# Performance work log

Measured on AMD Instinct MI355X. Metric: run time of the kernel, lower is better.

## Reference

```python
import jax, jax.numpy as jnp
import numpy as np

EPS = 1e-12  # torch F.normalize clamps the norm at 1e-12

def _l2norm(v, axis):
    n = jnp.sqrt(jnp.sum(v * v, axis=axis, keepdims=True))
    return v / jnp.maximum(n, EPS)

def setup_inputs() -> dict:
    key = jax.random.key(0)
    k1, k2, k3, k4 = jax.random.split(key, 4)
    N, C, H, W, K = 64, 64, 64, 64, 128
    alpha = 1.0
    x = jax.random.normal(k1, (N, C, H, W), dtype=jnp.float32)
    centroids = jax.random.uniform(k2, (K, C), dtype=jnp.float32)
    # conv is initialized from centroids (2*alpha*c, -alpha*||c||) but is an
    # independent parameter after init; keep the init relationship for realism.
    conv_w = 2.0 * alpha * centroids
    conv_b = -alpha * jnp.sqrt(jnp.sum(centroids * centroids, axis=1))
    return {"x": x, "centroids": centroids, "conv_w": conv_w, "conv_b": conv_b}

def reference(x, centroids, conv_w, conv_b):
    N, C, H, W = x.shape
    K = centroids.shape[0]
    # L2-normalize descriptors along channel dim
    xn = _l2norm(x, axis=1)                                   # [N,C,H,W]
    # 1x1 conv == per-pixel linear map C->K
    logits = jnp.einsum('nchw,kc->nkhw', xn, conv_w) + conv_b[None, :, None, None]
    sa = jax.nn.softmax(logits.reshape(N, K, H * W), axis=1)  # [N,K,HW]
    xf = xn.reshape(N, C, H * W)                              # [N,C,HW]
    # vlad[n,k,c] = sum_l sa[n,k,l] * (xf[n,c,l] - centroids[k,c])
    #            = (sa @ xf^T)[n,k,c] - sum_l sa[n,k,l] * centroids[k,c]
    vlad = jnp.einsum('nkl,ncl->nkc', sa, xf) - sa.sum(axis=-1)[:, :, None] * centroids[None]
    vlad = _l2norm(vlad, axis=2)            # intra-normalization per cluster
    vlad = vlad.reshape(N, K * C)
    vlad = _l2norm(vlad, axis=1)            # global L2 normalization
    return vlad
```

## Files before the change

### kernel.cpp

```cpp
#include <hip/hip_runtime.h>
#include <math.h>

#define NIMG   64
#define CDIM   64
#define HWPX   4096
#define KCL    128
#define TL     32
#define SHIFT  10.0f
#define RSQRT128 0.08838834764831845f

#define XP_S 72
#define XC_S 40
#define PH_S 40

typedef __attribute__((ext_vector_type(8))) short short8;
typedef __attribute__((ext_vector_type(4))) float f32x4;

#define MFMA(a, b, c) __builtin_amdgcn_mfma_f32_16x16x32_bf16((a), (b), (c), 0, 0, 0)

#define PERM_HI16 0x07060302u

#define BAR() do {                                          \
    asm volatile("s_waitcnt lgkmcnt(0)" ::: "memory");      \
    __builtin_amdgcn_s_barrier();                           \
    __builtin_amdgcn_sched_barrier(0);                      \
} while (0)

template <int NP>
__global__ __launch_bounds__(256, 2)
void netvlad_main(const float* __restrict__ x,
                  const float* __restrict__ conv_w,
                  const float* __restrict__ conv_b,
                  float* __restrict__ vout,
                  float* __restrict__ asout,
                  int use_atomic)
{
    constexpr int PIXPART = HWPX / NP;
    constexpr int NCHUNK  = PIXPART / TL;

    __shared__ __align__(16) short xp_hi[2][TL * XP_S], xp_lo[2][TL * XP_S];
    __shared__ __align__(16) short xc[2][CDIM * XC_S];
    __shared__ __align__(16) short ph[KCL * PH_S];
    __shared__ __align__(8) float2 redA2[2][4 * 16];
    __shared__ __align__(8) float2 sumP2[4 * 16];

    const int t   = threadIdx.x;
    const int w   = t >> 6;
    const int l   = t & 63;
    const int l15 = l & 15, l4 = l >> 4;
    const int n    = blockIdx.x / NP;
    const int part = blockIdx.x - n * NP;
    const int p_s  = t & 31;
    const int sg   = t >> 5;
    const int slot = 2 * (p_s & 15) + (p_s >> 4);

    short8 wh[2][2], wl[2][2];
    #pragma unroll
    for (int kt = 0; kt < 2; ++kt) {
        const int krow = (2 * w + kt) * 16 + l15;
        #pragma unroll
        for (int ks = 0; ks < 2; ++ks) {
            const float4* wp = (const float4*)(conv_w + krow * CDIM + ks * 32 + l4 * 8);
            float4 wa = wp[0], wb = wp[1];
            float wv[8] = {wa.x, wa.y, wa.z, wa.w, wb.x, wb.y, wb.z, wb.w};
            #pragma unroll
            for (int j = 0; j < 8; ++j) {
                unsigned u = __builtin_bit_cast(unsigned, wv[j]);
                wh[kt][ks][j] = (short)(u >> 16);
                float hf = __builtin_bit_cast(float, u & 0xffff0000u);
                wl[kt][ks][j] = (short)(__builtin_bit_cast(unsigned, wv[j] - hf) >> 16);
            }
        }
    }
    float cbr[2][4];
    #pragma unroll
    for (int kt = 0; kt < 2; ++kt)
        #pragma unroll
        for (int i = 0; i < 4; ++i)
            cbr[kt][i] = conv_b[(2 * w + kt) * 16 + l4 * 4 + i] - SHIFT;

    f32x4 acc2[2][4];
    #pragma unroll
    for (int a = 0; a < 2; ++a)
        #pragma unroll
        for (int b = 0; b < 4; ++b) acc2[a][b] = (f32x4)0.0f;
    float asr[2][4];
    #pragma unroll
    for (int a = 0; a < 2; ++a)
        #pragma unroll
        for (int i = 0; i < 4; ++i) asr[a][i] = 0.f;

    const float* xbase = x + (size_t)n * CDIM * HWPX + part * PIXPART;

    float xv[8];

    auto stage = [&](int buf) {
        float ssq = 0.f;
        #pragma unroll
        for (int j = 0; j < 8; ++j) ssq += xv[j] * xv[j];
        ssq += __shfl_xor(ssq, 32);
        float ssq_hi = __shfl_xor(ssq, 16);
        if (l < 16) redA2[buf][w * 16 + l15] = make_float2(ssq, ssq_hi);

        unsigned uh[4], ul[4];
        #pragma unroll
        for (int jp = 0; jp < 4; ++jp) {
            const unsigned u0 = __builtin_bit_cast(unsigned, xv[2 * jp]);
            const unsigned u1 = __builtin_bit_cast(unsigned, xv[2 * jp + 1]);
            uh[jp] = __builtin_amdgcn_perm(u1, u0, PERM_HI16);
            const float h0 = __builtin_bit_cast(float, u0 & 0xffff0000u);
            const float h1 = __builtin_bit_cast(float, u1 & 0xffff0000u);
            const unsigned lo0 = __builtin_bit_cast(unsigned, xv[2 * jp] - h0);
            const unsigned lo1 = __builtin_bit_cast(unsigned, xv[2 * jp + 1] - h1);
            ul[jp] = __builtin_amdgcn_perm(lo1, lo0, PERM_HI16);
        }
        *(uint4*)&xp_hi[buf][p_s * XP_S + sg * 8] = make_uint4(uh[0], uh[1], uh[2], uh[3]);
        *(uint4*)&xp_lo[buf][p_s * XP_S + sg * 8] = make_uint4(ul[0], ul[1], ul[2], ul[3]);

        #pragma unroll
        for (int jp = 0; jp < 4; ++jp) {
            unsigned pk;
            asm("v_cvt_pk_bf16_f32 %0, %1, %2"
                : "=v"(pk) : "v"(xv[2 * jp]), "v"(xv[2 * jp + 1]));
            xc[buf][(sg * 8 + 2 * jp)     * XC_S + slot] = (short)pk;
            xc[buf][(sg * 8 + 2 * jp + 1) * XC_S + slot] = (short)(pk >> 16);
        }
    };

    #pragma unroll
    for (int j = 0; j < 8; ++j)
        xv[j] = xbase[(sg * 8 + j) * HWPX + p_s];
    stage(0);
    if (NCHUNK > 1) {
        #pragma unroll
        for (int j = 0; j < 8; ++j)
            xv[j] = xbase[(sg * 8 + j) * HWPX + TL + p_s];
    }
    BAR();

    for (int ch = 0; ch < NCHUNK; ++ch) {
        const int cur = ch & 1;

        if (ch + 1 < NCHUNK) {
            stage(cur ^ 1);
            if (ch + 2 < NCHUNK) {
                #pragma unroll
                for (int j = 0; j < 8; ++j)
                    xv[j] = xbase[(sg * 8 + j) * HWPX + (ch + 2) * TL + p_s];
            }
        }

        f32x4 a1[2][2];
        #pragma unroll
        for (int a = 0; a < 2; ++a)
            #pragma unroll
            for (int b = 0; b < 2; ++b) a1[a][b] = (f32x4)0.0f;
        #pragma unroll
        for (int ks = 0; ks < 2; ++ks) {
            #pragma unroll
            for (int pt = 0; pt < 2; ++pt) {
                short8 bh = *(short8*)&xp_hi[cur][(pt * 16 + l15) * XP_S + ks * 32 + l4 * 8];
                short8 bl = *(short8*)&xp_lo[cur][(pt * 16 + l15) * XP_S + ks * 32 + l4 * 8];
                #pragma unroll
                for (int kt = 0; kt < 2; ++kt) {
                    a1[kt][pt] = MFMA(wh[kt][ks], bh, a1[kt][pt]);
                    a1[kt][pt] = MFMA(wh[kt][ks], bl, a1[kt][pt]);
                    a1[kt][pt] = MFMA(wl[kt][ks], bh, a1[kt][pt]);
                }
            }
        }

        float2 ra0 = redA2[cur][l15],      ra1 = redA2[cur][16 + l15];
        float2 ra2 = redA2[cur][32 + l15], ra3 = redA2[cur][48 + l15];
        float rn[2];
        rn[0] = 1.0f / fmaxf(sqrtf((ra0.x + ra1.x) + (ra2.x + ra3.x)), 1e-12f);
        rn[1] = 1.0f / fmaxf(sqrtf((ra0.y + ra1.y) + (ra2.y + ra3.y)), 1e-12f);

        float e[2][2][4], sp[2] = {0.f, 0.f};
        #pragma unroll
        for (int kt = 0; kt < 2; ++kt)
            #pragma unroll
            for (int pt = 0; pt < 2; ++pt)
                #pragma unroll
                for (int i = 0; i < 4; ++i) {
                    float ev = __expf(fmaf(a1[kt][pt][i], rn[pt], cbr[kt][i]));
                    e[kt][pt][i] = ev;
                    sp[pt] += ev;
                }
        #pragma unroll
        for (int pt = 0; pt < 2; ++pt) {
            sp[pt] += __shfl_xor(sp[pt], 16);
            sp[pt] += __shfl_xor(sp[pt], 32);
        }
        if (l4 == 0) sumP2[w * 16 + l15] = make_float2(sp[0], sp[1]);
        BAR();

        float2 q0 = sumP2[l15],      q1 = sumP2[16 + l15];
        float2 q2 = sumP2[32 + l15], q3 = sumP2[48 + l15];
        float rden[2], rdn2[2];
        rden[0] = 1.0f / ((q0.x + q1.x) + (q2.x + q3.x));
        rden[1] = 1.0f / ((q0.y + q1.y) + (q2.y + q3.y));
        rdn2[0] = rden[0] * rn[0];
        rdn2[1] = rden[1] * rn[1];

        #pragma unroll
        for (int kt = 0; kt < 2; ++kt)
            #pragma unroll
            for (int i = 0; i < 4; ++i) {
                const int row = (2 * w + kt) * 16 + l4 * 4 + i;
                const float e0 = e[kt][0][i], e1 = e[kt][1][i];
                asr[kt][i] = fmaf(e0, rden[0], asr[kt][i]);
                asr[kt][i] = fmaf(e1, rden[1], asr[kt][i]);
                const float p0 = e0 * rdn2[0], p1 = e1 * rdn2[1];
                unsigned pk;
                asm("v_cvt_pk_bf16_f32 %0, %1, %2" : "=v"(pk) : "v"(p0), "v"(p1));
                *(unsigned*)&ph[row * PH_S + 2 * l15] = pk;
            }

        {
            short8 xh2[4];
            #pragma unroll
            for (int ct = 0; ct < 4; ++ct)
                xh2[ct] = *(short8*)&xc[cur][(ct * 16 + l15) * XC_S + l4 * 8];
            #pragma unroll
            for (int kt = 0; kt < 2; ++kt) {
                short8 ah = *(short8*)&ph[((2 * w + kt) * 16 + l15) * PH_S + l4 * 8];
                #pragma unroll
                for (int ct = 0; ct < 4; ++ct)
                    acc2[kt][ct] = MFMA(ah, xh2[ct], acc2[kt][ct]);
            }
        }
        BAR();
    }

    float* vg = use_atomic ? vout + (size_t)n * KCL * CDIM
                           : vout + (size_t)blockIdx.x * KCL * CDIM;
    #pragma unroll
    for (int kt = 0; kt < 2; ++kt)
        #pragma unroll
        for (int ct = 0; ct < 4; ++ct)
            #pragma unroll
            for (int i = 0; i < 4; ++i) {
                const int row = (2 * w + kt) * 16 + l4 * 4 + i;
                const int col = ct * 16 + l15;
                if (use_atomic) atomicAdd(&vg[row * CDIM + col], acc2[kt][ct][i]);
                else            vg[row * CDIM + col] = acc2[kt][ct][i];
            }

    #pragma unroll
    for (int kt = 0; kt < 2; ++kt)
        #pragma unroll
        for (int i = 0; i < 4; ++i) {
            float v = asr[kt][i];
            v += __shfl_xor(v, 1); v += __shfl_xor(v, 2);
            v += __shfl_xor(v, 4); v += __shfl_xor(v, 8);
            if (l15 == 0) {
                const int row = (2 * w + kt) * 16 + l4 * 4 + i;
                if (use_atomic) atomicAdd(&asout[n * KCL + row], v);
                else            asout[blockIdx.x * KCL + row] = v;
            }
        }
}

__global__ __launch_bounds__(256)
void netvlad_finalize(const float* __restrict__ vpart,
                      const float* __restrict__ aspart,
                      const float* __restrict__ cent,
                      float* __restrict__ out,
                      int nparts)
{
    const int t = threadIdx.x;
    const int n  = blockIdx.x >> 3;
    const int kg = blockIdx.x & 7;
    const int k  = kg * 16 + (t >> 4);
    const int c0 = (t & 15) * 4;

    float vsum[4] = {0.f, 0.f, 0.f, 0.f};
    float av = 0.f;
    for (int pt = 0; pt < nparts; ++pt) {
        const float* vg = vpart + (((size_t)n * nparts + pt) * KCL + k) * CDIM + c0;
        float4 a = *(const float4*)vg;
        vsum[0] += a.x; vsum[1] += a.y; vsum[2] += a.z; vsum[3] += a.w;
        av += aspart[(n * nparts + pt) * KCL + k];
    }

    float4 cq = *(const float4*)(cent + k * CDIM + c0);
    float cc[4] = {cq.x, cq.y, cq.z, cq.w};
    float ss = 0.f;
    #pragma unroll
    for (int j = 0; j < 4; ++j) {
        vsum[j] -= av * cc[j];
        ss += vsum[j] * vsum[j];
    }
    ss += __shfl_xor(ss, 1); ss += __shfl_xor(ss, 2);
    ss += __shfl_xor(ss, 4); ss += __shfl_xor(ss, 8);
    const float s = (1.0f / fmaxf(sqrtf(ss), 1e-12f)) * RSQRT128;

    float4 o;
    o.x = vsum[0] * s; o.y = vsum[1] * s; o.z = vsum[2] * s; o.w = vsum[3] * s;
    *(float4*)(out + (size_t)n * KCL * CDIM + k * CDIM + c0) = o;
}

extern "C" void kernel_launch(void* const* d_in, const int* in_sizes, int n_in,
                              void* d_out, int out_size, void* d_ws, size_t ws_size,
                              hipStream_t stream) {
    const float* x     = (const float*)d_in[0];
    const float* cent  = (const float*)d_in[1];
    const float* convw = (const float*)d_in[2];
    const float* convb = (const float*)d_in[3];
    float* out = (float*)d_out;

    const size_t need8 = (size_t)NIMG * 8 * (KCL * CDIM + KCL) * sizeof(float);

    if (ws_size >= need8) {
        float* vws  = (float*)d_ws;
        float* asws = vws + (size_t)NIMG * 8 * KCL * CDIM;
        netvlad_main<8><<<dim3(NIMG * 8), dim3(256), 0, stream>>>(
            x, convw, convb, vws, asws, 0);
        netvlad_finalize<<<dim3(NIMG * 8), dim3(256), 0, stream>>>(
            vws, asws, cent, out, 8);
    } else {
        float* vws  = (float*)d_ws;
        float* asws = vws + (size_t)NIMG * KCL * CDIM;
        const size_t zb = (size_t)NIMG * (KCL * CDIM + KCL) * sizeof(float);
        hipMemsetAsync(d_ws, 0, zb, stream);
        netvlad_main<8><<<dim3(NIMG * 8), dim3(256), 0, stream>>>(
            x, convw, convb, vws, asws, 1);
        netvlad_finalize<<<dim3(NIMG * 8), dim3(256), 0, stream>>>(
            vws, asws, cent, out, 1);
    }
}
```

Before: 125.2 us.

## Double pixel chunk to 64 per iteration and halve barrier count

Raises the per-iteration pixel tile from 32 to 64, so each thread loads two pixel columns and each wave runs twice as many MFMAs between barriers. The loop body is restructured around this: the LDS strides, the norm and softmax-sum reduction layouts, and the second-stage MFMA over a 64-deep K dimension all change. The xc transpose store becomes a packed 32-bit write. The aim is fewer barriers and chunk iterations and better amortised LDS sync, at the cost of more registers and LDS, which may threaten 2 blocks per CU. The finalize kernel is also templated on the part count so its loop unrolls.

```diff
diff --git a/kernel.cpp b/kernel.cpp
--- a/kernel.cpp
+++ b/kernel.cpp
@@ -5,13 +5,13 @@
 #define CDIM   64
 #define HWPX   4096
 #define KCL    128
-#define TL     32
+#define TL     64
 #define SHIFT  10.0f
 #define RSQRT128 0.08838834764831845f
 
 #define XP_S 72
-#define XC_S 40
-#define PH_S 40
+#define XC_S 72
+#define PH_S 72
 
 typedef __attribute__((ext_vector_type(8))) short short8;
 typedef __attribute__((ext_vector_type(4))) float f32x4;
@@ -41,8 +41,8 @@
     __shared__ __align__(16) short xp_hi[2][TL * XP_S], xp_lo[2][TL * XP_S];
     __shared__ __align__(16) short xc[2][CDIM * XC_S];
     __shared__ __align__(16) short ph[KCL * PH_S];
-    __shared__ __align__(8) float2 redA2[2][4 * 16];
-    __shared__ __align__(8) float2 sumP2[4 * 16];
+    __shared__ __align__(8) float2 redA2[2][4 * 32];
+    __shared__ __align__(8) float2 sumP2[4 * 32];
 
     const int t   = threadIdx.x;
     const int w   = t >> 6;
@@ -50,9 +50,10 @@
     const int l15 = l & 15, l4 = l >> 4;
     const int n    = blockIdx.x / NP;
     const int part = blockIdx.x - n * NP;
-    const int p_s  = t & 31;
+    const int q    = t & 31;
     const int sg   = t >> 5;
-    const int slot = 2 * (p_s & 15) + (p_s >> 4);
+    const int p0   = (q & 15) + ((q & 16) << 1);
+    const int xslot = ((q >> 4) << 5) + 2 * (q & 15);
 
     short8 wh[2][2], wl[2][2];
     #pragma unroll
@@ -92,50 +93,72 @@
 
     const float* xbase = x + (size_t)n * CDIM * HWPX + part * PIXPART;
 
-    float xv[8];
+    float xv0[8], xv1[8];
+
+    #define LOADX(OFF) do {                                                 \
+        _Pragma("unroll")                                                   \
+        for (int j = 0; j < 8; ++j) {                                       \
+            xv0[j] = xbase[(sg * 8 + j) * HWPX + (OFF) + p0];               \
+            xv1[j] = xbase[(sg * 8 + j) * HWPX + (OFF) + p0 + 16];          \
+        }                                                                   \
+    } while (0)
 
     auto stage = [&](int buf) {
-        float ssq = 0.f;
-        #pragma unroll
-        for (int j = 0; j < 8; ++j) ssq += xv[j] * xv[j];
-        ssq += __shfl_xor(ssq, 32);
-        float ssq_hi = __shfl_xor(ssq, 16);
-        if (l < 16) redA2[buf][w * 16 + l15] = make_float2(ssq, ssq_hi);
-
-        unsigned uh[4], ul[4];
-        #pragma unroll
-        for (int jp = 0; jp < 4; ++jp) {
-            const unsigned u0 = __builtin_bit_cast(unsigned, xv[2 * jp]);
-            const unsigned u1 = __builtin_bit_cast(unsigned, xv[2 * jp + 1]);
-            uh[jp] = __builtin_amdgcn_perm(u1, u0, PERM_HI16);
-            const float h0 = __builtin_bit_cast(float, u0 & 0xffff0000u);
-            const float h1 = __builtin_bit_cast(float, u1 & 0xffff0000u);
-            const unsigned lo0 = __builtin_bit_cast(unsigned, xv[2 * jp] - h0);
-            const unsigned lo1 = __builtin_bit_cast(unsigned, xv[2 * jp + 1] - h1);
-            ul[jp] = __builtin_amdgcn_perm(lo1, lo0, PERM_HI16);
-        }
-        *(uint4*)&xp_hi[buf][p_s * XP_S + sg * 8] = make_uint4(uh[0], uh[1], uh[2], uh[3]);
-        *(uint4*)&xp_lo[buf][p_s * XP_S + sg * 8] = make_uint4(ul[0], ul[1], ul[2], ul[3]);
-
-        #pragma unroll
-        for (int jp = 0; jp < 4; ++jp) {
+        float ssq0 = 0.f, ssq1 = 0.f;
+        #pragma unroll
+        for (int j = 0; j < 8; ++j) {
+            ssq0 += xv0[j] * xv0[j];
+            ssq1 += xv1[j] * xv1[j];
+        }
+        ssq0 += __shfl_xor(ssq0, 32);
+        ssq1 += __shfl_xor(ssq1, 32);
+        if (l < 32) redA2[buf][w * 32 + q] = make_float2(ssq0, ssq1);
+
+        {
+            unsigned uh[4], ul[4];
+            #pragma unroll
+            for (int jp = 0; jp < 4; ++jp) {
+                const unsigned u0 = __builtin_bit_cast(unsigned, xv0[2 * jp]);
+                const unsigned u1 = __builtin_bit_cast(unsigned, xv0[2 * jp + 1]);
+                uh[jp] = __builtin_amdgcn_perm(u1, u0, PERM_HI16);
+                const float h0 = __builtin_bit_cast(float, u0 & 0xffff0000u);
+                const float h1 = __builtin_bit_cast(float, u1 & 0xffff0000u);
+                const unsigned lo0 = __builtin_bit_cast(unsigned, xv0[2 * jp] - h0);
+                const unsigned lo1 = __builtin_bit_cast(unsigned, xv0[2 * jp + 1] - h1);
+                ul[jp] = __builtin_amdgcn_perm(lo1, lo0, PERM_HI16);
+            }
+            *(uint4*)&xp_hi[buf][p0 * XP_S + sg * 8] = make_uint4(uh[0], uh[1], uh[2], uh[3]);
+            *(uint4*)&xp_lo[buf][p0 * XP_S + sg * 8] = make_uint4(ul[0], ul[1], ul[2], ul[3]);
+        }
+        {
+            unsigned uh[4], ul[4];
+            #pragma unroll
+            for (int jp = 0; jp < 4; ++jp) {
+                const unsigned u0 = __builtin_bit_cast(unsigned, xv1[2 * jp]);
+                const unsigned u1 = __builtin_bit_cast(unsigned, xv1[2 * jp + 1]);
+                uh[jp] = __builtin_amdgcn_perm(u1, u0, PERM_HI16);
+                const float h0 = __builtin_bit_cast(float, u0 & 0xffff0000u);
+                const float h1 = __builtin_bit_cast(float, u1 & 0xffff0000u);
+                const unsigned lo0 = __builtin_bit_cast(unsigned, xv1[2 * jp] - h0);
+                const unsigned lo1 = __builtin_bit_cast(unsigned, xv1[2 * jp + 1] - h1);
+                ul[jp] = __builtin_amdgcn_perm(lo1, lo0, PERM_HI16);
+            }
+            *(uint4*)&xp_hi[buf][(p0 + 16) * XP_S + sg * 8] = make_uint4(uh[0], uh[1], uh[2], uh[3]);
+            *(uint4*)&xp_lo[buf][(p0 + 16) * XP_S + sg * 8] = make_uint4(ul[0], ul[1], ul[2], ul[3]);
+        }
+
+        #pragma unroll
+        for (int j = 0; j < 8; ++j) {
             unsigned pk;
             asm("v_cvt_pk_bf16_f32 %0, %1, %2"
-                : "=v"(pk) : "v"(xv[2 * jp]), "v"(xv[2 * jp + 1]));
-            xc[buf][(sg * 8 + 2 * jp)     * XC_S + slot] = (short)pk;
-            xc[buf][(sg * 8 + 2 * jp + 1) * XC_S + slot] = (short)(pk >> 16);
+                : "=v"(pk) : "v"(xv0[j]), "v"(xv1[j]));
+            *(unsigned*)&xc[buf][(sg * 8 + j) * XC_S + xslot] = pk;
         }
     };
 
-    #pragma unroll
-    for (int j = 0; j < 8; ++j)
-        xv[j] = xbase[(sg * 8 + j) * HWPX + p_s];
+    LOADX(0);
     stage(0);
-    if (NCHUNK > 1) {
-        #pragma unroll
-        for (int j = 0; j < 8; ++j)
-            xv[j] = xbase[(sg * 8 + j) * HWPX + TL + p_s];
-    }
+    if (NCHUNK > 1) LOADX(TL);
     BAR();
 
     for (int ch = 0; ch < NCHUNK; ++ch) {
@@ -143,22 +166,18 @@
 
         if (ch + 1 < NCHUNK) {
             stage(cur ^ 1);
-            if (ch + 2 < NCHUNK) {
-                #pragma unroll
-                for (int j = 0; j < 8; ++j)
-                    xv[j] = xbase[(sg * 8 + j) * HWPX + (ch + 2) * TL + p_s];
-            }
-        }
-
-        f32x4 a1[2][2];
+            if (ch + 2 < NCHUNK) LOADX((ch + 2) * TL);
+        }
+
+        f32x4 a1[2][4];
         #pragma unroll
         for (int a = 0; a < 2; ++a)
             #pragma unroll
-            for (int b = 0; b < 2; ++b) a1[a][b] = (f32x4)0.0f;
+            for (int b = 0; b < 4; ++b) a1[a][b] = (f32x4)0.0f;
         #pragma unroll
         for (int ks = 0; ks < 2; ++ks) {
             #pragma unroll
-            for (int pt = 0; pt < 2; ++pt) {
+            for (int pt = 0; pt < 4; ++pt) {
                 short8 bh = *(short8*)&xp_hi[cur][(pt * 16 + l15) * XP_S + ks * 32 + l4 * 8];
                 short8 bl = *(short8*)&xp_lo[cur][(pt * 16 + l15) * XP_S + ks * 32 + l4 * 8];
                 #pragma unroll
@@ -170,17 +189,21 @@
             }
         }
 
-        float2 ra0 = redA2[cur][l15],      ra1 = redA2[cur][16 + l15];
-        float2 ra2 = redA2[cur][32 + l15], ra3 = redA2[cur][48 + l15];
-        float rn[2];
+        float2 ra0 = redA2[cur][l15],           ra1 = redA2[cur][32 + l15];
+        float2 ra2 = redA2[cur][64 + l15],      ra3 = redA2[cur][96 + l15];
+        float2 rb0 = redA2[cur][16 + l15],      rb1 = redA2[cur][48 + l15];
+        float2 rb2 = redA2[cur][80 + l15],      rb3 = redA2[cur][112 + l15];
+        float rn[4];
         rn[0] = 1.0f / fmaxf(sqrtf((ra0.x + ra1.x) + (ra2.x + ra3.x)), 1e-12f);
         rn[1] = 1.0f / fmaxf(sqrtf((ra0.y + ra1.y) + (ra2.y + ra3.y)), 1e-12f);
-
-        float e[2][2][4], sp[2] = {0.f, 0.f};
+        rn[2] = 1.0f / fmaxf(sqrtf((rb0.x + rb1.x) + (rb2.x + rb3.x)), 1e-12f);
+        rn[3] = 1.0f / fmaxf(sqrtf((rb0.y + rb1.y) + (rb2.y + rb3.y)), 1e-12f);
+
+        float e[2][4][4], sp[4] = {0.f, 0.f, 0.f, 0.f};
         #pragma unroll
         for (int kt = 0; kt < 2; ++kt)
             #pragma unroll
-            for (int pt = 0; pt < 2; ++pt)
+            for (int pt = 0; pt < 4; ++pt)
                 #pragma unroll
                 for (int i = 0; i < 4; ++i) {
                     float ev = __expf(fmaf(a1[kt][pt][i], rn[pt], cbr[kt][i]));
@@ -188,20 +211,25 @@
                     sp[pt] += ev;
                 }
         #pragma unroll
-        for (int pt = 0; pt < 2; ++pt) {
+        for (int pt = 0; pt < 4; ++pt) {
             sp[pt] += __shfl_xor(sp[pt], 16);
             sp[pt] += __shfl_xor(sp[pt], 32);
         }
-        if (l4 == 0) sumP2[w * 16 + l15] = make_float2(sp[0], sp[1]);
+        if (l4 == 0)      sumP2[w * 32 + l15]      = make_float2(sp[0], sp[1]);
+        else if (l4 == 1) sumP2[w * 32 + 16 + l15] = make_float2(sp[2], sp[3]);
         BAR();
 
-        float2 q0 = sumP2[l15],      q1 = sumP2[16 + l15];
-        float2 q2 = sumP2[32 + l15], q3 = sumP2[48 + l15];
-        float rden[2], rdn2[2];
+        float2 q0 = sumP2[l15],       q1 = sumP2[32 + l15];
+        float2 q2 = sumP2[64 + l15],  q3 = sumP2[96 + l15];
+        float2 r0 = sumP2[16 + l15],  r1 = sumP2[48 + l15];
+        float2 r2 = sumP2[80 + l15],  r3 = sumP2[112 + l15];
+        float rden[4], rdn2[4];
         rden[0] = 1.0f / ((q0.x + q1.x) + (q2.x + q3.x));
         rden[1] = 1.0f / ((q0.y + q1.y) + (q2.y + q3.y));
-        rdn2[0] = rden[0] * rn[0];
-        rdn2[1] = rden[1] * rn[1];
+        rden[2] = 1.0f / ((r0.x + r1.x) + (r2.x + r3.x));
+        rden[3] = 1.0f / ((r0.y + r1.y) + (r2.y + r3.y));
+        #pragma unroll
+        for (int pt = 0; pt < 4; ++pt) rdn2[pt] = rden[pt] * rn[pt];
 
         #pragma unroll
         for (int kt = 0; kt < 2; ++kt)
@@ -209,29 +237,41 @@
             for (int i = 0; i < 4; ++i) {
                 const int row = (2 * w + kt) * 16 + l4 * 4 + i;
                 const float e0 = e[kt][0][i], e1 = e[kt][1][i];
+                const float e2 = e[kt][2][i], e3 = e[kt][3][i];
                 asr[kt][i] = fmaf(e0, rden[0], asr[kt][i]);
                 asr[kt][i] = fmaf(e1, rden[1], asr[kt][i]);
-                const float p0 = e0 * rdn2[0], p1 = e1 * rdn2[1];
-                unsigned pk;
-                asm("v_cvt_pk_bf16_f32 %0, %1, %2" : "=v"(pk) : "v"(p0), "v"(p1));
-                *(unsigned*)&ph[row * PH_S + 2 * l15] = pk;
+                asr[kt][i] = fmaf(e2, rden[2], asr[kt][i]);
+                asr[kt][i] = fmaf(e3, rden[3], asr[kt][i]);
+                const float p0f = e0 * rdn2[0], p1f = e1 * rdn2[1];
+                const float p2f = e2 * rdn2[2], p3f = e3 * rdn2[3];
+                unsigned pk01, pk23;
+                asm("v_cvt_pk_bf16_f32 %0, %1, %2" : "=v"(pk01) : "v"(p0f), "v"(p1f));
+                asm("v_cvt_pk_bf16_f32 %0, %1, %2" : "=v"(pk23) : "v"(p2f), "v"(p3f));
+                *(unsigned*)&ph[row * PH_S + 2 * l15]      = pk01;
+                *(unsigned*)&ph[row * PH_S + 32 + 2 * l15] = pk23;
             }
 
         {
-            short8 xh2[4];
+            short8 xh2[4][2];
             #pragma unroll
             for (int ct = 0; ct < 4; ++ct)
-                xh2[ct] = *(short8*)&xc[cur][(ct * 16 + l15) * XC_S + l4 * 8];
+                #pragma unroll
+                for (int h = 0; h < 2; ++h)
+                    xh2[ct][h] = *(short8*)&xc[cur][(ct * 16 + l15) * XC_S + h * 32 + l4 * 8];
             #pragma unroll
             for (int kt = 0; kt < 2; ++kt) {
-                short8 ah = *(short8*)&ph[((2 * w + kt) * 16 + l15) * PH_S + l4 * 8];
+                short8 ah0 = *(short8*)&ph[((2 * w + kt) * 16 + l15) * PH_S + l4 * 8];
+                short8 ah1 = *(short8*)&ph[((2 * w + kt) * 16 + l15) * PH_S + 32 + l4 * 8];
                 #pragma unroll
-                for (int ct = 0; ct < 4; ++ct)
-                    acc2[kt][ct] = MFMA(ah, xh2[ct], acc2[kt][ct]);
+                for (int ct = 0; ct < 4; ++ct) {
+                    acc2[kt][ct] = MFMA(ah0, xh2[ct][0], acc2[kt][ct]);
+                    acc2[kt][ct] = MFMA(ah1, xh2[ct][1], acc2[kt][ct]);
+                }
             }
         }
         BAR();
     }
+    #undef LOADX
 
     float* vg = use_atomic ? vout + (size_t)n * KCL * CDIM
                            : vout + (size_t)blockIdx.x * KCL * CDIM;
@@ -262,12 +302,12 @@
         }
 }
 
+template <int NPARTS>
 __global__ __launch_bounds__(256)
 void netvlad_finalize(const float* __restrict__ vpart,
                       const float* __restrict__ aspart,
                       const float* __restrict__ cent,
-                      float* __restrict__ out,
-                      int nparts)
+                      float* __restrict__ out)
 {
     const int t = threadIdx.x;
     const int n  = blockIdx.x >> 3;
@@ -277,11 +317,12 @@
 
     float vsum[4] = {0.f, 0.f, 0.f, 0.f};
     float av = 0.f;
-    for (int pt = 0; pt < nparts; ++pt) {
-        const float* vg = vpart + (((size_t)n * nparts + pt) * KCL + k) * CDIM + c0;
+    #pragma unroll
+    for (int pt = 0; pt < NPARTS; ++pt) {
+        const float* vg = vpart + (((size_t)n * NPARTS + pt) * KCL + k) * CDIM + c0;
         float4 a = *(const float4*)vg;
         vsum[0] += a.x; vsum[1] += a.y; vsum[2] += a.z; vsum[3] += a.w;
-        av += aspart[(n * nparts + pt) * KCL + k];
+        av += aspart[(n * NPARTS + pt) * KCL + k];
     }
 
     float4 cq = *(const float4*)(cent + k * CDIM + c0);
@@ -317,8 +358,8 @@
         float* asws = vws + (size_t)NIMG * 8 * KCL * CDIM;
         netvlad_main<8><<<dim3(NIMG * 8), dim3(256), 0, stream>>>(
             x, convw, convb, vws, asws, 0);
-        netvlad_finalize<<<dim3(NIMG * 8), dim3(256), 0, stream>>>(
-            vws, asws, cent, out, 8);
+        netvlad_finalize<8><<<dim3(NIMG * 8), dim3(256), 0, stream>>>(
+            vws, asws, cent, out);
     } else {
         float* vws  = (float*)d_ws;
         float* asws = vws + (size_t)NIMG * KCL * CDIM;
@@ -326,7 +367,7 @@
         hipMemsetAsync(d_ws, 0, zb, stream);
         netvlad_main<8><<<dim3(NIMG * 8), dim3(256), 0, stream>>>(
             x, convw, convb, vws, asws, 1);
-        netvlad_finalize<<<dim3(NIMG * 8), dim3(256), 0, stream>>>(
-            vws, asws, cent, out, 1);
+        netvlad_finalize<1><<<dim3(NIMG * 8), dim3(256), 0, stream>>>(
+            vws, asws, cent, out);
     }
 }
```

Result: faster. 122.1 us, median of 2 (-2.5%).
